# Kernel tuning notes

Measured on AMD Instinct MI355X. Metric: run time of the kernel, lower is better.

The kernel has to match this reference:

```python
import jax, jax.numpy as jnp
import numpy as np

B, T, F, H, C = 1024, 64, 256, 1024, 2


def setup_inputs() -> dict:
    key = jax.random.key(0)
    ks = jax.random.split(key, 16)
    s = 1.0 / np.sqrt(H)
    return {
        "X": jax.random.normal(ks[0], (B, T, F), jnp.float32),
        "missing_mask": (jax.random.uniform(ks[1], (B, T, F)) > 0.3).astype(jnp.float32),
        "deltas": jax.random.uniform(ks[2], (B, T, F), jnp.float32) * 5.0,
        "empirical_mean": jax.random.normal(ks[3], (B, F), jnp.float32),
        "X_filledLOCF": jax.random.normal(ks[4], (B, T, F), jnp.float32),
        # TemporalDecay h: full linear F->H
        "w_gh": jax.random.normal(ks[5], (H, F), jnp.float32) * 0.02,
        "b_gh": jnp.zeros((H,), jnp.float32),
        # TemporalDecay x: diagonal (W masked by identity) -> vector of size F
        "w_gx": jax.random.normal(ks[6], (F,), jnp.float32) * 0.02,
        "b_gx": jnp.zeros((F,), jnp.float32),
        # GRUCell: input size 2F+H, hidden H
        "w_ih": jax.random.uniform(ks[7], (3 * H, 2 * F + H), jnp.float32, -s, s),
        "w_hh": jax.random.uniform(ks[8], (3 * H, H), jnp.float32, -s, s),
        "b_ih": jax.random.uniform(ks[9], (3 * H,), jnp.float32, -s, s),
        "b_hh": jax.random.uniform(ks[10], (3 * H,), jnp.float32, -s, s),
        # classifier H -> C
        "w_cls": jax.random.normal(ks[11], (C, H), jnp.float32) * 0.02,
        "b_cls": jnp.zeros((C,), jnp.float32),
    }


def _grud_forward(X, missing_mask, deltas, empirical_mean, X_filledLOCF,
                  w_gh, b_gh, w_gx, b_gx, w_ih, w_hh, b_ih, b_hh, w_cls, b_cls):
    # time-major for scan: [T, B, F]
    Xt = jnp.swapaxes(X, 0, 1)
    Mt = jnp.swapaxes(missing_mask, 0, 1)
    Dt = jnp.swapaxes(deltas, 0, 1)
    Lt = jnp.swapaxes(X_filledLOCF, 0, 1)

    def step(h, xs):
        x, m, d, x_locf = xs
        # TemporalDecay: gamma = exp(-relu(W d + b))
        gamma_h = jnp.exp(-jax.nn.relu(d @ w_gh.T + b_gh))        # [B, H]
        gamma_x = jnp.exp(-jax.nn.relu(d * w_gx + b_gx))          # [B, F] (diag)
        h = h * gamma_h
        x_h = gamma_x * x_locf + (1.0 - gamma_x) * empirical_mean
        x_replaced = m * x + (1.0 - m) * x_h
        inp = jnp.concatenate([x_replaced, h, m], axis=1)         # [B, 2F+H]
        # GRUCell
        gi = inp @ w_ih.T + b_ih                                   # [B, 3H]
        gh = h @ w_hh.T + b_hh                                     # [B, 3H]
        i_r, i_z, i_n = jnp.split(gi, 3, axis=1)
        h_r, h_z, h_n = jnp.split(gh, 3, axis=1)
        r = jax.nn.sigmoid(i_r + h_r)
        z = jax.nn.sigmoid(i_z + h_z)
        n = jnp.tanh(i_n + r * h_n)
        h_new = (1.0 - z) * n + z * h
        return h_new, None

    h0 = jnp.zeros((X.shape[0], w_hh.shape[1]), X.dtype)
    h_final, _ = jax.lax.scan(step, h0, (Xt, Mt, Dt, Lt))
    logits = h_final @ w_cls.T + b_cls
    return jax.nn.softmax(logits, axis=1)


def reference(X, missing_mask, deltas, empirical_mean, X_filledLOCF,
              w_gh, b_gh, w_gx, b_gx, w_ih, w_hh, b_ih, b_hh, w_cls, b_cls):
    return _grud_forward(X, missing_mask, deltas, empirical_mean, X_filledLOCF,
                         w_gh, b_gh, w_gx, b_gx, w_ih, w_hh, b_ih, b_hh, w_cls, b_cls)
```

## Files before the change

### kernel.cpp

```cpp
#include <hip/hip_runtime.h>

using bf16   = __bf16;
using bf16x8 = __bf16 __attribute__((ext_vector_type(8)));
using f32x4  = float  __attribute__((ext_vector_type(4)));


__device__ __forceinline__ float sigm(float x) { return 1.f / (1.f + __expf(-x)); }
__device__ __forceinline__ float tanh_fast(float x) {
  float e = __expf(2.f * x);
  return 1.f - 2.f / (e + 1.f);
}

#define GLL16(gsrc, ldst)                                                              \
  __builtin_amdgcn_global_load_lds((const __attribute__((address_space(1))) void*)(gsrc), \
                                   (__attribute__((address_space(3))) void*)(ldst), 16, 0, 0)

__global__ void prep_kernel(const float* __restrict__ X, const float* __restrict__ Msk,
                            const float* __restrict__ D, const float* __restrict__ Mean,
                            const float* __restrict__ L, const float* __restrict__ w_gx,
                            const float* __restrict__ b_gx,
                            bf16* __restrict__ XRs, bf16* __restrict__ Dbfs,
                            int c, int nsl) {
  int i = blockIdx.x * 256 + threadIdx.x;
  if (i >= (nsl << 18)) return;
  int f = i & 255, b = (i >> 8) & 1023, tl = i >> 18;
  int t = c * 16 + tl;
  size_t g = ((size_t)b << 14) + ((size_t)t << 8) + f;
  float d = D[g];
  int fs = f ^ ((b & 7) << 3);
  int row = tl * 1024 + b;
  Dbfs[(size_t)row * 256 + fs] = (bf16)d;
  float gx = __expf(-fmaxf(d * w_gx[f] + b_gx[f], 0.f));
  float xh = gx * L[g] + (1.f - gx) * Mean[(size_t)b * 256 + f];
  float m  = Msk[g];
  float xr = m * X[g] + (1.f - m) * xh;
  if (tl < 16) {
    size_t xo = (size_t)row * 512;
    XRs[xo + fs]       = (bf16)xr;
    XRs[xo + 256 + fs] = (bf16)m;
  }
}

__global__ void wprep_kernel(const float* __restrict__ w_ih, const float* __restrict__ w_hh,
                             const float* __restrict__ b_ih, const float* __restrict__ b_hh,
                             const float* __restrict__ w_gh,
                             bf16* __restrict__ WcH3, bf16* __restrict__ WcX3,
                             bf16* __restrict__ Wgs, float* __restrict__ bias4) {
  int i = blockIdx.x * 256 + threadIdx.x;
  if (i < 4194304) {
    int blk = i >> 13;
    int nb = blk >> 4, kt = blk & 15;
    int r = i & 8191;
    int nl = r >> 6, cc = (r >> 3) & 7, e = r & 7;
    int gg = nl >> 5, j = nb * 32 + (nl & 31);
    int k = kt * 64 + ((cc ^ (nl & 7)) << 3) + e;
    float v;
    if (gg == 3) v = w_hh[(size_t)(2048 + j) * 1024 + k];
    else {
      int rr = gg * 1024 + j;
      v = w_ih[(size_t)rr * 1536 + 256 + k];
      if (gg < 2) v += w_hh[(size_t)rr * 1024 + k];
    }
    WcH3[i] = (bf16)v;
  } else if (i < 5767168) {
    int q = i - 4194304;
    int blk = q >> 13;
    int nb = blk >> 3, kt = blk & 7;
    int r = q & 8191;
    int nl = r >> 6, cc = (r >> 3) & 7, e = r & 7;
    int gg = nb >> 3;
    int j  = (nb & 7) * 128 + nl;
    int rr = gg * 1024 + j;
    int k = kt * 64 + ((cc ^ (nl & 7)) << 3) + e;
    float v = (k < 256) ? w_ih[(size_t)rr * 1536 + k]
                        : w_ih[(size_t)rr * 1536 + 1280 + (k - 256)];
    WcX3[q] = (bf16)v;
  } else if (i < 6029312) {
    int q = i - 5767168;
    int blk = q >> 13;
    int nb = blk >> 2, kt = blk & 3;
    int r = q & 8191;
    int nl = r >> 6, cc = (r >> 3) & 7, e = r & 7;
    int n = nb * 128 + nl;
    int k = kt * 64 + ((cc ^ (nl & 7)) << 3) + e;
    Wgs[q] = (bf16)w_gh[(size_t)n * 256 + k];
  } else if (i < 6033408) {
    int q = i - 6029312;
    int gg = q >> 10, j = q & 1023;
    float v;
    if (gg == 0)      v = b_ih[j] + b_hh[j];
    else if (gg == 1) v = b_ih[1024 + j] + b_hh[1024 + j];
    else if (gg == 2) v = b_ih[2048 + j];
    else              v = b_hh[2048 + j];
    bias4[q] = v;
  }
}

__global__ __launch_bounds__(256) void gammah_kernel(const bf16* __restrict__ Dbfs,
                                                     const bf16* __restrict__ Wgs,
                                                     const float* __restrict__ b_gh,
                                                     bf16* __restrict__ GH) {
  __shared__ char smem[65536];
  char* As = smem;
  char* Bs = smem + 32768;
  int tid = threadIdx.x, lane = tid & 63, wid = tid >> 6;
  int wr = wid >> 1, wc = wid & 1;
  int cpx = gridDim.x >> 3;
  int wg = (blockIdx.x & 7) * cpx + (blockIdx.x >> 3);
  int nb = wg & 7, mb = wg >> 3;

  const bf16* aA = Dbfs + ((size_t)(mb * 128 + wid * 8 + (lane >> 3))) * 256 + (lane & 7) * 8;
  const bf16* aB = Wgs + (size_t)nb * 4 * 8192 + wid * 512 + lane * 8;

  f32x4 acc[4][4];
#pragma unroll
  for (int a = 0; a < 4; ++a)
#pragma unroll
    for (int b = 0; b < 4; ++b)
#pragma unroll
      for (int q = 0; q < 4; ++q) acc[a][b][q] = 0.f;

#define GM_STAGE(buf, kt)                                                         \
  do {                                                                            \
    _Pragma("unroll")                                                             \
    for (int q = 0; q < 4; ++q)                                                   \
      GLL16(aA + q * (32 * 256) + (kt) * 64, As + (buf) * 16384 + (q * 4 + wid) * 1024); \
    _Pragma("unroll")                                                             \
    for (int q = 0; q < 4; ++q)                                                   \
      GLL16(aB + (size_t)(kt) * 8192 + q * 2048, Bs + (buf) * 16384 + (q * 4 + wid) * 1024); \
  } while (0)

  GM_STAGE(0, 0);
  __syncthreads();
  for (int kt = 0; kt < 4; ++kt) {
    const int cur = kt & 1;
    if (kt < 3) GM_STAGE(cur ^ 1, kt + 1);
#pragma unroll
    for (int kk = 0; kk < 2; ++kk) {
      int kb = kk * 64 + ((lane >> 4) << 4);
      bf16x8 af[4], bfr[4];
#pragma unroll
      for (int mf = 0; mf < 4; ++mf) {
        int row = wr * 64 + mf * 16 + (lane & 15);
        af[mf] = *(const bf16x8*)(As + cur * 16384 + (((row * 128 + kb)) ^ ((row & 7) << 4)));
      }
#pragma unroll
      for (int nf = 0; nf < 4; ++nf) {
        int nl = wc * 64 + nf * 16 + (lane & 15);
        bfr[nf] = *(const bf16x8*)(Bs + cur * 16384 + (((nl * 128 + kb)) ^ ((nl & 7) << 4)));
      }
#pragma unroll
      for (int mf = 0; mf < 4; ++mf)
#pragma unroll
        for (int nf = 0; nf < 4; ++nf)
          acc[mf][nf] = __builtin_amdgcn_mfma_f32_16x16x32_bf16(af[mf], bfr[nf], acc[mf][nf], 0, 0, 0);
    }
    __syncthreads();
  }
  char* ep = smem;
#pragma unroll
  for (int nf = 0; nf < 4; ++nf) {
    int col = wc * 64 + nf * 16 + (lane & 15);
    float bg = b_gh[nb * 128 + col];
#pragma unroll
    for (int mf = 0; mf < 4; ++mf)
#pragma unroll
      for (int reg = 0; reg < 4; ++reg) {
        int row = wr * 64 + mf * 16 + ((lane >> 4) << 2) + reg;
        int cph = ((col >> 3) ^ (((row >> 2) & 3) << 2));
        *(bf16*)(ep + row * 256 + (cph << 4) + (col & 7) * 2) =
            (bf16)__expf(-fmaxf(acc[mf][nf][reg] + bg, 0.f));
      }
  }
  __syncthreads();
#pragma unroll
  for (int p = 0; p < 8; ++p) {
    int idx = p * 256 + tid;
    int row = idx >> 4, c = idx & 15;
    int cph = c ^ (((row >> 2) & 3) << 2);
    bf16x8 v = *(const bf16x8*)(ep + row * 256 + (cph << 4));
    *(bf16x8*)(GH + (size_t)(mb * 128 + row) * 1024 + nb * 128 + c * 8) = v;
  }
}

__global__ __launch_bounds__(256) void gix_kernel(const bf16* __restrict__ XRs,
                                                  const bf16* __restrict__ WcX3,
                                                  bf16* __restrict__ Gi) {
  __shared__ char smem[65536];
  char* As = smem;
  char* Bs = smem + 32768;
  int tid = threadIdx.x, lane = tid & 63, wid = tid >> 6;
  int wr = wid >> 1, wc = wid & 1;
  int cpx = gridDim.x >> 3;
  int wg = (blockIdx.x & 7) * cpx + (blockIdx.x >> 3);
  int nb = wg % 24, mb = wg / 24;

  const bf16* aA = XRs + ((size_t)(mb * 128 + wid * 8 + (lane >> 3))) * 512 + (lane & 7) * 8;
  const bf16* aB = WcX3 + (size_t)nb * 8 * 8192 + wid * 512 + lane * 8;

  f32x4 acc[4][4];
#pragma unroll
  for (int a = 0; a < 4; ++a)
#pragma unroll
    for (int b = 0; b < 4; ++b)
#pragma unroll
      for (int q = 0; q < 4; ++q) acc[a][b][q] = 0.f;

#define GX_STAGE(buf, kt)                                                         \
  do {                                                                            \
    _Pragma("unroll")                                                             \
    for (int q = 0; q < 4; ++q)                                                   \
      GLL16(aA + q * (32 * 512) + (kt) * 64, As + (buf) * 16384 + (q * 4 + wid) * 1024); \
    _Pragma("unroll")                                                             \
    for (int q = 0; q < 4; ++q)                                                   \
      GLL16(aB + (size_t)(kt) * 8192 + q * 2048, Bs + (buf) * 16384 + (q * 4 + wid) * 1024); \
  } while (0)

  GX_STAGE(0, 0);
  __syncthreads();
  for (int kt = 0; kt < 8; ++kt) {
    const int cur = kt & 1;
    if (kt < 7) GX_STAGE(cur ^ 1, kt + 1);
#pragma unroll
    for (int kk = 0; kk < 2; ++kk) {
      int kb = kk * 64 + ((lane >> 4) << 4);
      bf16x8 af[4], bfr[4];
#pragma unroll
      for (int mf = 0; mf < 4; ++mf) {
        int row = wr * 64 + mf * 16 + (lane & 15);
        af[mf] = *(const bf16x8*)(As + cur * 16384 + (((row * 128 + kb)) ^ ((row & 7) << 4)));
      }
#pragma unroll
      for (int nf = 0; nf < 4; ++nf) {
        int nl = wc * 64 + nf * 16 + (lane & 15);
        bfr[nf] = *(const bf16x8*)(Bs + cur * 16384 + (((nl * 128 + kb)) ^ ((nl & 7) << 4)));
      }
#pragma unroll
      for (int mf = 0; mf < 4; ++mf)
#pragma unroll
        for (int nf = 0; nf < 4; ++nf)
          acc[mf][nf] = __builtin_amdgcn_mfma_f32_16x16x32_bf16(af[mf], bfr[nf], acc[mf][nf], 0, 0, 0);
    }
    __syncthreads();
  }
  char* ep = smem;
#pragma unroll
  for (int nf = 0; nf < 4; ++nf) {
    int col = wc * 64 + nf * 16 + (lane & 15);
#pragma unroll
    for (int mf = 0; mf < 4; ++mf)
#pragma unroll
      for (int reg = 0; reg < 4; ++reg) {
        int row = wr * 64 + mf * 16 + ((lane >> 4) << 2) + reg;
        int cph = ((col >> 3) ^ (((row >> 2) & 3) << 2));
        *(bf16*)(ep + row * 256 + (cph << 4) + (col & 7) * 2) = (bf16)acc[mf][nf][reg];
      }
  }
  __syncthreads();
  {
    int sl = mb >> 3, mbl = mb & 7;
    bf16* plane = Gi + (size_t)sl * 3145728 + (size_t)(nb >> 3) * 1048576 + (nb & 7) * 128;
#pragma unroll
    for (int p = 0; p < 8; ++p) {
      int idx = p * 256 + tid;
      int row = idx >> 4, c = idx & 15;
      int cph = c ^ (((row >> 2) & 3) << 2);
      bf16x8 v = *(const bf16x8*)(ep + row * 256 + (cph << 4));
      *(bf16x8*)(plane + (size_t)(mbl * 128 + row) * 1024 + c * 8) = v;
    }
  }
}

__global__ __launch_bounds__(512) void step_kernel(
    const bf16* __restrict__ hbs, const float* __restrict__ hf,
    const bf16* __restrict__ WcH3, const float* __restrict__ bias4,
    const bf16* __restrict__ gi, const bf16* __restrict__ gh_next, int is_last,
    float* __restrict__ hf_next, bf16* __restrict__ hbs_next) {
  __shared__ char smem[49152];
  int tid = threadIdx.x, lane = tid & 63, wid = tid >> 6;
  int wr = wid >> 1, wc = wid & 1;
  int wg = ((blockIdx.x & 7) << 6) + (blockIdx.x >> 3);
  int mb = wg & 15, nb = wg >> 4;

  const bf16* aA = hbs + ((size_t)(mb * 64 + (tid >> 3))) * 1024 + (tid & 7) * 8;
  const bf16* aB = WcH3 + (size_t)nb * 131072 + tid * 8;

  int j = nb * 32 + wc * 16 + (lane & 15);
  bf16  grv[4], gzv[4], gnv[4], ghv[4];
  float hfv[4];
#pragma unroll
  for (int reg = 0; reg < 4; ++reg) {
    int brow = mb * 64 + wr * 16 + ((lane >> 4) << 2) + reg;
    size_t hb_ = (size_t)brow * 1024 + j;
    grv[reg] = gi[hb_];
    gzv[reg] = gi[1048576 + hb_];
    gnv[reg] = gi[2097152 + hb_];
    ghv[reg] = gh_next[hb_];
    hfv[reg] = hf[hb_];
  }

  f32x4 acc[4];
#pragma unroll
  for (int b = 0; b < 4; ++b)
#pragma unroll
    for (int q = 0; q < 4; ++q) acc[b][q] = 0.f;

#define ST_STAGE(buf, kt)                                                         \
  do {                                                                            \
    GLL16(aA + (kt) * 64,                 smem + (buf) * 8192 + wid * 1024);      \
    GLL16(aB + (kt) * 8192,               smem + 16384 + (buf) * 16384 + wid * 1024); \
    GLL16(aB + (kt) * 8192 + 4096,        smem + 16384 + (buf) * 16384 + 8192 + wid * 1024); \
  } while (0)

  ST_STAGE(0, 0);
  for (int kt = 0; kt < 16; ++kt) {
    const int cur = kt & 1;
    if (kt < 15) {
      ST_STAGE(cur ^ 1, kt + 1);
      asm volatile("s_waitcnt vmcnt(3)" ::: "memory");
    } else {
      asm volatile("s_waitcnt vmcnt(0)" ::: "memory");
    }
    __builtin_amdgcn_sched_barrier(0);
    __builtin_amdgcn_s_barrier();
    __builtin_amdgcn_sched_barrier(0);
    const char* Ab = smem + cur * 8192;
    const char* Bb = smem + 16384 + cur * 16384;
#pragma unroll
    for (int kk = 0; kk < 2; ++kk) {
      int kb = kk * 64 + ((lane >> 4) << 4);
      int row = wr * 16 + (lane & 15);
      bf16x8 af = *(const bf16x8*)(Ab + (((row * 128 + kb)) ^ ((row & 7) << 4)));
      bf16x8 bfr[4];
#pragma unroll
      for (int g = 0; g < 4; ++g) {
        int nl = g * 32 + wc * 16 + (lane & 15);
        bfr[g] = *(const bf16x8*)(Bb + (((nl * 128 + kb)) ^ ((nl & 7) << 4)));
      }
#pragma unroll
      for (int g = 0; g < 4; ++g)
        acc[g] = __builtin_amdgcn_mfma_f32_16x16x32_bf16(af, bfr[g], acc[g], 0, 0, 0);
    }
    asm volatile("s_waitcnt lgkmcnt(0)" ::: "memory");
    __builtin_amdgcn_sched_barrier(0);
    __builtin_amdgcn_s_barrier();
  }

  float br = bias4[j], bz = bias4[1024 + j], bn = bias4[2048 + j], bh = bias4[3072 + j];
#pragma unroll
  for (int reg = 0; reg < 4; ++reg) {
    int brow = mb * 64 + wr * 16 + ((lane >> 4) << 2) + reg;
    float pr  = acc[0][reg] + (float)grv[reg] + br;
    float pz  = acc[1][reg] + (float)gzv[reg] + bz;
    float pin = acc[2][reg] + (float)gnv[reg] + bn;
    float phn = acc[3][reg] + bh;
    float r = sigm(pr), z = sigm(pz);
    float nn = tanh_fast(pin + r * phn);
    float hnew = (1.f - z) * nn + z * hfv[reg];
    float gam = is_last ? 1.f : (float)ghv[reg];
    float hd = hnew * gam;
    hf_next[(size_t)brow * 1024 + j] = hd;
    hbs_next[(size_t)brow * 1024 + (j ^ ((brow & 7) << 3))] = (bf16)hd;
  }
}

__global__ void cls_kernel(const float* __restrict__ h, const float* __restrict__ w_cls,
                           const float* __restrict__ b_cls, float* __restrict__ out) {
  int wid = threadIdx.x >> 6, lane = threadIdx.x & 63;
  int b = blockIdx.x * 4 + wid;
  const float* hb = h + (size_t)b * 1024;
  float a0 = 0.f, a1 = 0.f;
#pragma unroll
  for (int e = 0; e < 16; ++e) {
    int i = e * 64 + lane;
    float hv = hb[i];
    a0 += hv * w_cls[i];
    a1 += hv * w_cls[1024 + i];
  }
  for (int off = 32; off; off >>= 1) {
    a0 += __shfl_down(a0, off);
    a1 += __shfl_down(a1, off);
  }
  if (lane == 0) {
    float l0 = a0 + b_cls[0], l1 = a1 + b_cls[1];
    float mx = fmaxf(l0, l1);
    float e0 = __expf(l0 - mx), e1 = __expf(l1 - mx);
    float s = e0 + e1;
    out[b * 2]     = e0 / s;
    out[b * 2 + 1] = e1 / s;
  }
}

extern "C" void kernel_launch(void* const* d_in, const int* in_sizes, int n_in,
                              void* d_out, int out_size, void* d_ws, size_t ws_size,
                              hipStream_t stream) {
  const float* X     = (const float*)d_in[0];
  const float* Msk   = (const float*)d_in[1];
  const float* D     = (const float*)d_in[2];
  const float* Mean  = (const float*)d_in[3];
  const float* L     = (const float*)d_in[4];
  const float* w_gh  = (const float*)d_in[5];
  const float* b_gh  = (const float*)d_in[6];
  const float* w_gx  = (const float*)d_in[7];
  const float* b_gx  = (const float*)d_in[8];
  const float* w_ih  = (const float*)d_in[9];
  const float* w_hh  = (const float*)d_in[10];
  const float* b_ih  = (const float*)d_in[11];
  const float* b_hh  = (const float*)d_in[12];
  const float* w_cls = (const float*)d_in[13];
  const float* b_cls = (const float*)d_in[14];

  char* w = (char*)d_ws;
  bf16*  XRs   = (bf16*)(w);
  bf16*  Dbfs  = (bf16*)(w + 16777216);
  bf16*  GH    = (bf16*)(w + 25690112);
  bf16*  WcX3  = (bf16*)(w + 61341696);
  bf16*  WcH3  = (bf16*)(w + 65536000);
  bf16*  Wgs   = (bf16*)(w + 73924608);
  float* bias4 = (float*)(w + 74448896);
  float* hf0   = (float*)(w + 74465280);
  float* hf1   = (float*)(w + 78659584);
  bf16*  hb0   = (bf16*)(w + 82853888);
  bf16*  hb1   = (bf16*)(w + 84951040);
  bf16*  Gi    = (bf16*)(w + 87048192);

  size_t base = 87048192;
  int GCH = 16;
  while (GCH > 1 && base + (size_t)GCH * 6291456ull > ws_size) GCH >>= 1;

  float* hfp[2] = {hf0, hf1};
  bf16*  hbp[2] = {hb0, hb1};

  hipMemsetAsync(hf0, 0, 4194304, stream);
  hipMemsetAsync(hb0, 0, 2097152, stream);
  wprep_kernel<<<23568, 256, 0, stream>>>(w_ih, w_hh, b_ih, b_hh, w_gh, WcH3, WcX3, Wgs, bias4);

  int t = 0;
  for (int c = 0; c < 4; ++c) {
    int nsl = (c < 3) ? 17 : 16;
    prep_kernel<<<nsl * 1024, 256, 0, stream>>>(X, Msk, D, Mean, L, w_gx, b_gx, XRs, Dbfs, c, nsl);
    gammah_kernel<<<nsl * 64, 256, 0, stream>>>(Dbfs, Wgs, b_gh, GH);
    for (int sub = 0; sub < 16 / GCH; ++sub) {
      gix_kernel<<<GCH * 192, 256, 0, stream>>>(XRs + (size_t)sub * GCH * 524288, WcX3, Gi);
      for (int tl2 = 0; tl2 < GCH; ++tl2, ++t) {
        int tl = sub * GCH + tl2;
        int cur = t & 1, nxt = cur ^ 1;
        step_kernel<<<512, 512, 0, stream>>>(
            hbp[cur], hfp[cur], WcH3, bias4,
            Gi + (size_t)tl2 * 3145728, GH + (size_t)(tl + 1) * 1048576,
            (t == 63) ? 1 : 0, hfp[nxt], hbp[nxt]);
      }
    }
  }
  cls_kernel<<<256, 256, 0, stream>>>(hfp[0], w_cls, b_cls, (float*)d_out);
}
```

Measured before the change: 1.387 ms.

## Retile recurrent step GEMM to 2x4 warps with lane-shuffle gate gather; slice gammah

The per-timestep GRU kernel now arranges its 8 warps as 2x4 instead of 4x2. Each warp computes a 32x32 tile using 2x2 MFMA fragments, so every A fragment serves two B fragments, and the gate columns are interleaved across lanes. Partial gate results are exchanged with __shfl_xor so each lane ends up with all four gates for its output element. Separately, the gamma_h GEMM kernel is rewritten to work on a per-slice grid with single-buffered 32KB LDS, dropping its double-buffer prefetch, likely so it can run alongside other work with higher occupancy. This trades load overlap for lower LDS use and adds shuffle overhead in the epilogue.

```diff
diff --git a/kernel.cpp b/kernel.cpp
--- a/kernel.cpp
+++ b/kernel.cpp
@@ -100,17 +100,16 @@
                                                      const bf16* __restrict__ Wgs,
                                                      const float* __restrict__ b_gh,
                                                      bf16* __restrict__ GH) {
-  __shared__ char smem[65536];
+  __shared__ char smem[32768];
   char* As = smem;
-  char* Bs = smem + 32768;
+  char* Bs = smem + 16384;
   int tid = threadIdx.x, lane = tid & 63, wid = tid >> 6;
   int wr = wid >> 1, wc = wid & 1;
-  int cpx = gridDim.x >> 3;
-  int wg = (blockIdx.x & 7) * cpx + (blockIdx.x >> 3);
-  int nb = wg & 7, mb = wg >> 3;
-
-  const bf16* aA = Dbfs + ((size_t)(mb * 128 + wid * 8 + (lane >> 3))) * 256 + (lane & 7) * 8;
-  const bf16* aB = Wgs + (size_t)nb * 4 * 8192 + wid * 512 + lane * 8;
+  int slice = blockIdx.x >> 6, sub = blockIdx.x & 63;
+  int mb = sub >> 3, nb = sub & 7;
+
+  const bf16* aA = Dbfs + ((size_t)(slice * 1024 + mb * 128 + wid * 8 + (lane >> 3))) * 256 + (lane & 7) * 8;
+  const bf16* aB = Wgs + (size_t)nb * 32768 + wid * 512 + lane * 8;
 
   f32x4 acc[4][4];
 #pragma unroll
@@ -120,21 +119,14 @@
 #pragma unroll
       for (int q = 0; q < 4; ++q) acc[a][b][q] = 0.f;
 
-#define GM_STAGE(buf, kt)                                                         \
-  do {                                                                            \
-    _Pragma("unroll")                                                             \
-    for (int q = 0; q < 4; ++q)                                                   \
-      GLL16(aA + q * (32 * 256) + (kt) * 64, As + (buf) * 16384 + (q * 4 + wid) * 1024); \
-    _Pragma("unroll")                                                             \
-    for (int q = 0; q < 4; ++q)                                                   \
-      GLL16(aB + (size_t)(kt) * 8192 + q * 2048, Bs + (buf) * 16384 + (q * 4 + wid) * 1024); \
-  } while (0)
-
-  GM_STAGE(0, 0);
-  __syncthreads();
   for (int kt = 0; kt < 4; ++kt) {
-    const int cur = kt & 1;
-    if (kt < 3) GM_STAGE(cur ^ 1, kt + 1);
+#pragma unroll
+    for (int q = 0; q < 4; ++q)
+      GLL16(aA + q * (32 * 256) + kt * 64, As + (q * 4 + wid) * 1024);
+#pragma unroll
+    for (int q = 0; q < 4; ++q)
+      GLL16(aB + kt * 8192 + q * 2048, Bs + (q * 4 + wid) * 1024);
+    __syncthreads();
 #pragma unroll
     for (int kk = 0; kk < 2; ++kk) {
       int kb = kk * 64 + ((lane >> 4) << 4);
@@ -142,12 +134,12 @@
 #pragma unroll
       for (int mf = 0; mf < 4; ++mf) {
         int row = wr * 64 + mf * 16 + (lane & 15);
-        af[mf] = *(const bf16x8*)(As + cur * 16384 + (((row * 128 + kb)) ^ ((row & 7) << 4)));
+        af[mf] = *(const bf16x8*)(As + (((row * 128 + kb)) ^ ((row & 7) << 4)));
       }
 #pragma unroll
       for (int nf = 0; nf < 4; ++nf) {
         int nl = wc * 64 + nf * 16 + (lane & 15);
-        bfr[nf] = *(const bf16x8*)(Bs + cur * 16384 + (((nl * 128 + kb)) ^ ((nl & 7) << 4)));
+        bfr[nf] = *(const bf16x8*)(Bs + (((nl * 128 + kb)) ^ ((nl & 7) << 4)));
       }
 #pragma unroll
       for (int mf = 0; mf < 4; ++mf)
@@ -179,7 +171,7 @@
     int row = idx >> 4, c = idx & 15;
     int cph = c ^ (((row >> 2) & 3) << 2);
     bf16x8 v = *(const bf16x8*)(ep + row * 256 + (cph << 4));
-    *(bf16x8*)(GH + (size_t)(mb * 128 + row) * 1024 + nb * 128 + c * 8) = v;
+    *(bf16x8*)(GH + (size_t)(slice * 1024 + mb * 128 + row) * 1024 + nb * 128 + c * 8) = v;
   }
 }
 
@@ -278,19 +270,21 @@
     float* __restrict__ hf_next, bf16* __restrict__ hbs_next) {
   __shared__ char smem[49152];
   int tid = threadIdx.x, lane = tid & 63, wid = tid >> 6;
-  int wr = wid >> 1, wc = wid & 1;
+  int wr = wid >> 2, wc = wid & 3;
   int wg = ((blockIdx.x & 7) << 6) + (blockIdx.x >> 3);
   int mb = wg & 15, nb = wg >> 4;
 
   const bf16* aA = hbs + ((size_t)(mb * 64 + (tid >> 3))) * 1024 + (tid & 7) * 8;
   const bf16* aB = WcH3 + (size_t)nb * 131072 + tid * 8;
 
-  int j = nb * 32 + wc * 16 + (lane & 15);
+  int mSel = (lane >> 3) & 1;
+  int j = nb * 32 + wc * 8 + (lane & 7);
+
   bf16  grv[4], gzv[4], gnv[4], ghv[4];
   float hfv[4];
 #pragma unroll
   for (int reg = 0; reg < 4; ++reg) {
-    int brow = mb * 64 + wr * 16 + ((lane >> 4) << 2) + reg;
+    int brow = mb * 64 + wr * 32 + mSel * 16 + ((lane >> 4) << 2) + reg;
     size_t hb_ = (size_t)brow * 1024 + j;
     grv[reg] = gi[hb_];
     gzv[reg] = gi[1048576 + hb_];
@@ -299,11 +293,13 @@
     hfv[reg] = hf[hb_];
   }
 
-  f32x4 acc[4];
-#pragma unroll
-  for (int b = 0; b < 4; ++b)
-#pragma unroll
-    for (int q = 0; q < 4; ++q) acc[b][q] = 0.f;
+  f32x4 acc[2][2];
+#pragma unroll
+  for (int a = 0; a < 2; ++a)
+#pragma unroll
+    for (int b = 0; b < 2; ++b)
+#pragma unroll
+      for (int q = 0; q < 4; ++q) acc[a][b][q] = 0.f;
 
 #define ST_STAGE(buf, kt)                                                         \
   do {                                                                            \
@@ -329,31 +325,49 @@
 #pragma unroll
     for (int kk = 0; kk < 2; ++kk) {
       int kb = kk * 64 + ((lane >> 4) << 4);
-      int row = wr * 16 + (lane & 15);
-      bf16x8 af = *(const bf16x8*)(Ab + (((row * 128 + kb)) ^ ((row & 7) << 4)));
-      bf16x8 bfr[4];
-#pragma unroll
-      for (int g = 0; g < 4; ++g) {
-        int nl = g * 32 + wc * 16 + (lane & 15);
-        bfr[g] = *(const bf16x8*)(Bb + (((nl * 128 + kb)) ^ ((nl & 7) << 4)));
-      }
-#pragma unroll
-      for (int g = 0; g < 4; ++g)
-        acc[g] = __builtin_amdgcn_mfma_f32_16x16x32_bf16(af, bfr[g], acc[g], 0, 0, 0);
+      bf16x8 af[2], bfr[2];
+#pragma unroll
+      for (int m = 0; m < 2; ++m) {
+        int row = wr * 32 + m * 16 + (lane & 15);
+        af[m] = *(const bf16x8*)(Ab + (((row * 128 + kb)) ^ ((row & 7) << 4)));
+      }
+#pragma unroll
+      for (int f = 0; f < 2; ++f) {
+        int nl = (f * 2 + ((lane & 15) >> 3)) * 32 + wc * 8 + (lane & 7);
+        bfr[f] = *(const bf16x8*)(Bb + (((nl * 128 + kb)) ^ ((nl & 7) << 4)));
+      }
+#pragma unroll
+      for (int m = 0; m < 2; ++m)
+#pragma unroll
+        for (int f = 0; f < 2; ++f)
+          acc[m][f] = __builtin_amdgcn_mfma_f32_16x16x32_bf16(af[m], bfr[f], acc[m][f], 0, 0, 0);
     }
     asm volatile("s_waitcnt lgkmcnt(0)" ::: "memory");
     __builtin_amdgcn_sched_barrier(0);
     __builtin_amdgcn_s_barrier();
   }
 
+  float sh00[4], sh01[4], sh10[4], sh11[4];
+#pragma unroll
+  for (int q = 0; q < 4; ++q) {
+    sh00[q] = __shfl_xor(acc[0][0][q], 8);
+    sh01[q] = __shfl_xor(acc[0][1][q], 8);
+    sh10[q] = __shfl_xor(acc[1][0][q], 8);
+    sh11[q] = __shfl_xor(acc[1][1][q], 8);
+  }
+  int hi = mSel;
   float br = bias4[j], bz = bias4[1024 + j], bn = bias4[2048 + j], bh = bias4[3072 + j];
 #pragma unroll
   for (int reg = 0; reg < 4; ++reg) {
-    int brow = mb * 64 + wr * 16 + ((lane >> 4) << 2) + reg;
-    float pr  = acc[0][reg] + (float)grv[reg] + br;
-    float pz  = acc[1][reg] + (float)gzv[reg] + bz;
-    float pin = acc[2][reg] + (float)gnv[reg] + bn;
-    float phn = acc[3][reg] + bh;
+    float g0 = hi ? sh10[reg]      : acc[0][0][reg];
+    float g1 = hi ? acc[1][0][reg] : sh00[reg];
+    float g2 = hi ? sh11[reg]      : acc[0][1][reg];
+    float g3 = hi ? acc[1][1][reg] : sh01[reg];
+    int brow = mb * 64 + wr * 32 + mSel * 16 + ((lane >> 4) << 2) + reg;
+    float pr  = g0 + (float)grv[reg] + br;
+    float pz  = g1 + (float)gzv[reg] + bz;
+    float pin = g2 + (float)gnv[reg] + bn;
+    float phn = g3 + bh;
     float r = sigm(pr), z = sigm(pz);
     float nn = tanh_fast(pin + r * phn);
     float hnew = (1.f - z) * nn + z * hfv[reg];
```

Measured after the change: 1.430 ms. 1.03x slower.
